# Performance work log

Measured on AMD Instinct MI355X. Metric: run time of the kernel, lower is better.

## Reference

```python
import jax, jax.numpy as jnp
import numpy as np
import math

HID, NH, NKV, HD = 2048, 16, 4, 128
GROUPS = NH // NKV

def fq(x, bits, axis=None):
    # symmetric fake-quant with straight-through rounding; per-tensor unless axis given
    qmax = 2.0 ** (bits - 1) - 1.0
    if axis is None:
        amax = jnp.max(jnp.abs(x))
    else:
        amax = jnp.max(jnp.abs(x), axis=axis, keepdims=True)
    scale = jnp.maximum(amax, 1e-8) / qmax
    q = jnp.clip(jnp.round(x / scale), -qmax - 1.0, qmax) * scale
    return x + jax.lax.stop_gradient(q - x)

def dyn_quant_linear(x, W, b, w_bits=8):
    # DynamicQuantLinear: per-out-channel weight fake-quant + dynamic per-tensor 8-bit act quant
    Wq = fq(W, w_bits, axis=1)          # W: [out, in]
    xq = fq(x, 8)
    y = xq @ Wq.T
    return y + b if b is not None else y

def fq_matmul(a, b, a_bits, b_bits):
    # FakeQuantMatmul
    return jnp.einsum('hqd,hdk->hqk', fq(a, a_bits), fq(b, b_bits))

def rotate_half(x):
    x1, x2 = jnp.split(x, 2, axis=-1)
    return jnp.concatenate([-x2, x1], axis=-1)

def setup_inputs() -> dict:
    key = jax.random.key(0)
    ks = jax.random.split(key, 12)
    inp = {
        'hidden_states': jax.random.normal(ks[0], (1, 512, HID), jnp.float32),
        'cos': jax.random.uniform(ks[1], (1, 512, HD), jnp.float32),
        'sin': jax.random.uniform(ks[2], (1, 512, HD), jnp.float32),
        'cache_k': jax.random.normal(ks[3], (NKV, 8192, HD), jnp.float32),
        'cache_v': jax.random.normal(ks[4], (NKV, 8192, HD), jnp.float32),
        'mask': jnp.zeros((1, 512, 8192), jnp.float32),
        'Wq': jax.random.normal(ks[5], (NH * HD, HID), jnp.float32) * 0.02,
        'bq': jnp.zeros((NH * HD,), jnp.float32),
        'Wk': jax.random.normal(ks[6], (NKV * HD, HID), jnp.float32) * 0.02,
        'bk': jnp.zeros((NKV * HD,), jnp.float32),
        'Wv': jax.random.normal(ks[7], (NKV * HD, HID), jnp.float32) * 0.02,
        'bv': jnp.zeros((NKV * HD,), jnp.float32),
        'Wo': jax.random.normal(ks[8], (HID, NH * HD), jnp.float32) * 0.02,
    }
    return inp

def reference(hidden_states, cos, sin, cache_k, cache_v, mask, Wq, bq, Wk, bk, Wv, bv, Wo):
    # ConstFakeQuant on incoming caches
    cache_k = fq(cache_k, 8)
    cache_v = fq(cache_v, 8)
    seqlen = hidden_states.shape[1]
    x = hidden_states.reshape(seqlen, HID)  # batch_size == 1
    q = dyn_quant_linear(x, Wq, bq).reshape(seqlen, NH, HD).transpose(1, 0, 2)    # [NH,S,D]
    k = dyn_quant_linear(x, Wk, bk).reshape(seqlen, NKV, HD).transpose(1, 0, 2)   # [NKV,S,D]
    v = dyn_quant_linear(x, Wv, bv).reshape(seqlen, NKV, HD).transpose(1, 0, 2)   # [NKV,S,D]
    # RoPE
    q = q * cos + rotate_half(q) * sin
    k = k * cos + rotate_half(k) * sin
    c_len = cache_k.shape[1]
    # sliding KV cache: drop oldest seqlen, append new
    cache_k = jnp.concatenate([cache_k[:, seqlen:, :], k], axis=1)   # [NKV,c_len,D]
    cache_v = jnp.concatenate([cache_v[:, seqlen:, :], v], axis=1)
    kT = cache_k.transpose(0, 2, 1)                                   # [NKV,D,c_len]
    q4 = q.reshape(NKV, GROUPS * seqlen, HD)
    attn = fq_matmul(q4, kT, 8, 8)                                    # [NKV,G*S,c_len]
    attn = attn.reshape(NH, seqlen, c_len) / math.sqrt(HD)
    attn = attn + mask
    attn = jax.nn.softmax(attn, axis=-1)
    attn = attn.reshape(NKV, GROUPS * seqlen, c_len)
    out = fq_matmul(attn, cache_v, 8, 8)                              # sv: [NKV,G*S,D]
    out = out.reshape(NH, seqlen, HD).transpose(1, 0, 2).reshape(1, seqlen, HID)
    out = dyn_quant_linear(out.reshape(seqlen, HID), Wo, None).reshape(1, seqlen, HID)
    # cache outputs re-fake-quantized
    k_out = fq(k, 8)
    v_out = fq(v, 8)
    return (out, k_out, v_out)
```

## Files before the change

kernel.cpp:

```cpp
#include <hip/hip_runtime.h>
#include <math.h>

#define S_LEN 512
#define HID 2048
#define NH 16
#define NKV 4
#define HD 128
#define CL 8192
#define TAILN (CL - S_LEN)
#define NKO (NKV * S_LEN * HD)
#define KS1 16
#define KCH1 (CL / KS1)
#define KS2 8
#define KCH2 (CL / KS2)
#define INV_SQRT_HD 0.08838834764831845f

typedef unsigned short u16;
typedef unsigned int u32;
typedef __attribute__((ext_vector_type(8))) unsigned short u16x8;
typedef __attribute__((ext_vector_type(4))) unsigned short u16x4;
typedef __attribute__((ext_vector_type(8))) short bf16x8;
typedef __attribute__((ext_vector_type(4))) float f32x4;

enum {
  SC_AMAX_X = 0, SC_AMAX_CK, SC_AMAX_CK_TAIL, SC_AMAX_CV, SC_AMAX_CV_TAIL,
  SC_AMAX_Q, SC_AMAX_K, SC_AMAX_V, SC_AMAX_AO, SC_MIN_L,
  SC_NUM
};

__device__ __forceinline__ float warpMax64(float v) {
  #pragma unroll
  for (int o = 32; o; o >>= 1) v = fmaxf(v, __shfl_down(v, o, 64));
  return v;
}
__device__ __forceinline__ float warpMin64(float v) {
  #pragma unroll
  for (int o = 32; o; o >>= 1) v = fminf(v, __shfl_down(v, o, 64));
  return v;
}
__device__ __forceinline__ float blockMax256(float v) {
  __shared__ float sm_[4];
  __syncthreads();
  v = warpMax64(v);
  if ((threadIdx.x & 63) == 0) sm_[threadIdx.x >> 6] = v;
  __syncthreads();
  return fmaxf(fmaxf(sm_[0], sm_[1]), fmaxf(sm_[2], sm_[3]));
}
__device__ __forceinline__ float blockMin256(float v) {
  __shared__ float sn_[4];
  __syncthreads();
  v = warpMin64(v);
  if ((threadIdx.x & 63) == 0) sn_[threadIdx.x >> 6] = v;
  __syncthreads();
  return fminf(fminf(sn_[0], sn_[1]), fminf(sn_[2], sn_[3]));
}
__device__ __forceinline__ void atomicMinPosF(float* a, float v) {
  atomicMin((unsigned int*)a, __float_as_uint(v));
}
__device__ __forceinline__ float clampq(float q) {
  return fminf(fmaxf(q, -128.f), 127.f);
}
__device__ __forceinline__ u16 bf16bits(float f) {
  return (u16)(__float_as_uint(f) >> 16);
}
__device__ __forceinline__ float mk_scale(float am) {
  return fmaxf(am, 1e-8f) / 127.f;
}
__device__ __forceinline__ void gl2lds16(const u16* g, u16* l) {
  __builtin_amdgcn_global_load_lds((const __attribute__((address_space(1))) void*)g,
                                   (__attribute__((address_space(3))) void*)l, 16, 0, 0);
}

__global__ __launch_bounds__(256) void k_pre(const float* __restrict__ hidden,
                                             const float* __restrict__ ck, const float* __restrict__ cv,
                                             float* __restrict__ pp) {
  int b = blockIdx.x, tid = threadIdx.x;
  if (b < 512) {
    const int n4 = S_LEN * HID / 4;
    float m = 0.f;
    const float4* x4 = (const float4*)hidden;
    for (int i = b * 256 + tid; i < n4; i += 512 * 256) {
      float4 v = x4[i];
      m = fmaxf(m, fmaxf(fmaxf(fabsf(v.x), fabsf(v.y)), fmaxf(fabsf(v.z), fabsf(v.w))));
    }
    m = blockMax256(m);
    if (tid == 0) pp[b] = m;
  } else {
    int isv = b >= 1024;
    int bb = b - (isv ? 1024 : 512);
    const float4* x4 = (const float4*)(isv ? cv : ck);
    const int n4 = NKV * CL * HD / 4;
    float mf = 0.f, mt = 0.f;
    for (int i = bb * 256 + tid; i < n4; i += 512 * 256) {
      float4 v = x4[i];
      float a = fmaxf(fmaxf(fabsf(v.x), fabsf(v.y)), fmaxf(fabsf(v.z), fabsf(v.w)));
      mf = fmaxf(mf, a);
      int t = (i >> 5) & (CL - 1);
      if (t >= S_LEN) mt = fmaxf(mt, a);
    }
    mf = blockMax256(mf);
    mt = blockMax256(mt);
    if (tid == 0) {
      pp[512 + isv * 1024 + bb] = mf;
      pp[1024 + isv * 1024 + bb] = mt;
    }
  }
}

__global__ __launch_bounds__(256) void k_reduce_pre(const float* __restrict__ pp, float* __restrict__ sc) {
  const int slots[5] = {SC_AMAX_X, SC_AMAX_CK, SC_AMAX_CK_TAIL, SC_AMAX_CV, SC_AMAX_CV_TAIL};
  if (threadIdx.x == 0) sc[SC_MIN_L] = INFINITY;
  #pragma unroll
  for (int r = 0; r < 5; r++) {
    float v = fmaxf(pp[r * 512 + threadIdx.x], pp[r * 512 + 256 + threadIdx.x]);
    v = blockMax256(v);
    if (threadIdx.x == 0) sc[slots[r]] = v;
  }
}

__global__ __launch_bounds__(256) void k_quant_w_all(const float* __restrict__ Wq, const float* __restrict__ Wk,
                                                     const float* __restrict__ Wv, const float* __restrict__ Wo,
                                                     u16* __restrict__ WQb, u16* __restrict__ WKb,
                                                     u16* __restrict__ WVb, u16* __restrict__ WOb,
                                                     float* __restrict__ SWq, float* __restrict__ SWk,
                                                     float* __restrict__ SWv, float* __restrict__ SWo) {
  int r = blockIdx.x;
  const float* W; u16* Wb; float* SW; int row;
  if (r < 2048)      { W = Wq; Wb = WQb; SW = SWq; row = r; }
  else if (r < 2560) { W = Wk; Wb = WKb; SW = SWk; row = r - 2048; }
  else if (r < 3072) { W = Wv; Wb = WVb; SW = SWv; row = r - 2560; }
  else               { W = Wo; Wb = WOb; SW = SWo; row = r - 3072; }
  size_t base = (size_t)row * HID;
  const float4* w4 = (const float4*)(W + base);
  int tid = threadIdx.x;
  float4 va = w4[tid];
  float4 vb = w4[tid + 256];
  float am = fmaxf(fmaxf(fmaxf(fabsf(va.x), fabsf(va.y)), fmaxf(fabsf(va.z), fabsf(va.w))),
                   fmaxf(fmaxf(fabsf(vb.x), fabsf(vb.y)), fmaxf(fabsf(vb.z), fabsf(vb.w))));
  am = blockMax256(am);
  float s = fmaxf(am, 1e-8f) / 127.f;
  if (tid == 0) SW[row] = s;
  u16x4 oa, ob;
  oa[0] = bf16bits(clampq(rintf(va.x / s)));
  oa[1] = bf16bits(clampq(rintf(va.y / s)));
  oa[2] = bf16bits(clampq(rintf(va.z / s)));
  oa[3] = bf16bits(clampq(rintf(va.w / s)));
  ob[0] = bf16bits(clampq(rintf(vb.x / s)));
  ob[1] = bf16bits(clampq(rintf(vb.y / s)));
  ob[2] = bf16bits(clampq(rintf(vb.z / s)));
  ob[3] = bf16bits(clampq(rintf(vb.w / s)));
  *(u16x4*)(Wb + base + (size_t)tid * 4) = oa;
  *(u16x4*)(Wb + base + (size_t)(tid + 256) * 4) = ob;
}

__global__ __launch_bounds__(256) void k_quant_act_b(const float* __restrict__ in, u16* __restrict__ outp,
                                                     int n4, const float* __restrict__ sc, int axslot) {
  float s = mk_scale(sc[axslot]);
  const float4* i4 = (const float4*)in;
  for (int i = blockIdx.x * 256 + threadIdx.x; i < n4; i += gridDim.x * 256) {
    float4 v = i4[i];
    u16x4 o;
    o[0] = bf16bits(clampq(rintf(v.x / s)));
    o[1] = bf16bits(clampq(rintf(v.y / s)));
    o[2] = bf16bits(clampq(rintf(v.z / s)));
    o[3] = bf16bits(clampq(rintf(v.w / s)));
    *(u16x4*)(outp + (size_t)i * 4) = o;
  }
}

__global__ __launch_bounds__(256) void k_quant_q(const float* __restrict__ QB, u16* __restrict__ QI,
                                                 const float* __restrict__ sc) {
  int idx = blockIdx.x * 256 + threadIdx.x;
  float s = mk_scale(sc[SC_AMAX_Q]);
  int e = idx * 4;
  int srow = e >> 11, rem = e & 2047;
  int h = rem >> 7, d = rem & 127;
  float4 v = *(const float4*)&QB[e];
  u16x4 o;
  o[0] = bf16bits(clampq(rintf(v.x / s)));
  o[1] = bf16bits(clampq(rintf(v.y / s)));
  o[2] = bf16bits(clampq(rintf(v.z / s)));
  o[3] = bf16bits(clampq(rintf(v.w / s)));
  *(u16x4*)(QI + ((size_t)h * S_LEN + srow) * HD + d) = o;
}

#define GQ_STAGE(BUF, K0)                                                          \
  {                                                                                \
    _Pragma("unroll")                                                              \
    for (int i = 0; i < 2; i++) {                                                  \
      int b = tid + i * 256;                                                       \
      int row = b >> 3, c8d = b & 7, c8s = c8d ^ (row & 7);                        \
      gl2lds16(A + (size_t)(r0 + row) * HID + (K0) + c8s * 8, Al[BUF] + b * 8);    \
    }                                                                              \
    _Pragma("unroll")                                                              \
    for (int i = 0; i < 2; i++) {                                                  \
      int b = tid + i * 256;                                                       \
      int row = b >> 3, c8d = b & 7, c8s = c8d ^ (row & 7);                        \
      gl2lds16(B + (size_t)(c0 + row) * HID + (K0) + c8s * 8, Bl[BUF] + b * 8);    \
    }                                                                              \
  }

#define GQ_TILE(BUF)                                                               \
  {                                                                                \
    _Pragma("unroll")                                                              \
    for (int ks = 0; ks < 2; ks++) {                                               \
      bf16x8 af[2], bfr[2];                                                        \
      _Pragma("unroll")                                                            \
      for (int a = 0; a < 2; a++) {                                                \
        int row = wy * 32 + a * 16 + c;                                            \
        af[a] = *(const bf16x8*)(Al[BUF] + row * 64 + (((4 * ks + g) ^ (row & 7)) * 8)); \
      }                                                                            \
      _Pragma("unroll")                                                            \
      for (int b2 = 0; b2 < 2; b2++) {                                             \
        int row = wx * 32 + b2 * 16 + c;                                           \
        bfr[b2] = *(const bf16x8*)(Bl[BUF] + row * 64 + (((4 * ks + g) ^ (row & 7)) * 8)); \
      }                                                                            \
      _Pragma("unroll")                                                            \
      for (int a = 0; a < 2; a++)                                                  \
        _Pragma("unroll")                                                          \
        for (int b2 = 0; b2 < 2; b2++)                                             \
          acc[a][b2] = __builtin_amdgcn_mfma_f32_16x16x32_bf16(af[a], bfr[b2], acc[a][b2], 0, 0, 0); \
    }                                                                              \
  }

__global__ __launch_bounds__(256) void k_gemm_qkv(const u16* __restrict__ A,
                                                  const u16* __restrict__ WQb, const u16* __restrict__ WKb,
                                                  const u16* __restrict__ WVb,
                                                  const float* __restrict__ SWq, const float* __restrict__ SWk,
                                                  const float* __restrict__ SWv,
                                                  const float* __restrict__ bq, const float* __restrict__ bk,
                                                  const float* __restrict__ bv,
                                                  const float* __restrict__ sc,
                                                  float* __restrict__ QB, float* __restrict__ KB,
                                                  float* __restrict__ VB) {
  __shared__ u16 Al[2][64 * 64];
  __shared__ u16 Bl[2][64 * 64];
  int bx = blockIdx.x;
  const u16* B; const float* SW; const float* bias; float* C; int N, c0;
  if (bx < 32)      { B = WQb; SW = SWq; bias = bq; C = QB; N = HID; c0 = bx * 64; }
  else if (bx < 40) { B = WKb; SW = SWk; bias = bk; C = KB; N = NKV * HD; c0 = (bx - 32) * 64; }
  else              { B = WVb; SW = SWv; bias = bv; C = VB; N = NKV * HD; c0 = (bx - 40) * 64; }
  int tid = threadIdx.x, lane = tid & 63, w = tid >> 6;
  int g = lane >> 4, c = lane & 15;
  int wy = w >> 1, wx = w & 1;
  int r0 = blockIdx.y * 64;
  float sx = mk_scale(sc[SC_AMAX_X]);
  f32x4 acc[2][2] = {};
  GQ_STAGE(0, 0)
  __syncthreads();
  for (int k0 = 0; k0 < HID; k0 += 128) {
    GQ_STAGE(1, k0 + 64)
    GQ_TILE(0)
    __syncthreads();
    if (k0 + 128 < HID) GQ_STAGE(0, k0 + 128)
    GQ_TILE(1)
    __syncthreads();
  }
  #pragma unroll
  for (int a = 0; a < 2; a++)
    #pragma unroll
    for (int b2 = 0; b2 < 2; b2++) {
      int col = c0 + wx * 32 + b2 * 16 + c;
      float sca = sx * SW[col];
      float bs = bias[col];
      #pragma unroll
      for (int r = 0; r < 4; r++) {
        int row = r0 + wy * 32 + a * 16 + 4 * g + r;
        C[(size_t)row * N + col] = acc[a][b2][r] * sca + bs;
      }
    }
}

__global__ __launch_bounds__(256) void k_gemm_q(const u16* __restrict__ A, const u16* __restrict__ B,
                                                const float* __restrict__ SW, const float* __restrict__ sc,
                                                int axslot, float* __restrict__ C, int M, int N, int K) {
  __shared__ u16 Al[2][64 * 64];
  __shared__ u16 Bl[2][64 * 64];
  int tid = threadIdx.x, lane = tid & 63, w = tid >> 6;
  int g = lane >> 4, c = lane & 15;
  int wy = w >> 1, wx = w & 1;
  int r0 = blockIdx.y * 64, c0 = blockIdx.x * 64;
  float sx = mk_scale(sc[axslot]);
  f32x4 acc[2][2] = {};
  GQ_STAGE(0, 0)
  __syncthreads();
  for (int k0 = 0; k0 < HID; k0 += 128) {
    GQ_STAGE(1, k0 + 64)
    GQ_TILE(0)
    __syncthreads();
    if (k0 + 128 < HID) GQ_STAGE(0, k0 + 128)
    GQ_TILE(1)
    __syncthreads();
  }
  #pragma unroll
  for (int a = 0; a < 2; a++)
    #pragma unroll
    for (int b2 = 0; b2 < 2; b2++) {
      int col = c0 + wx * 32 + b2 * 16 + c;
      float sca = sx * SW[col];
      #pragma unroll
      for (int r = 0; r < 4; r++) {
        int row = r0 + wy * 32 + a * 16 + 4 * g + r;
        C[(size_t)row * N + col] = acc[a][b2][r] * sca;
      }
    }
}

__global__ __launch_bounds__(256) void k_rope_amax(float* __restrict__ QB, float* __restrict__ KB,
                                                   const float* __restrict__ VB,
                                                   const float* __restrict__ cosb, const float* __restrict__ sinb,
                                                   float* __restrict__ PR) {
  const int nQ = S_LEN * NH * 64;
  const int nK = S_LEN * NKV * 64;
  int idx = blockIdx.x * 256 + threadIdx.x;
  float am = 0.f;
  if (idx < nQ) {
    int s = idx >> 10, rem = idx & 1023, h = rem >> 6, d = rem & 63;
    float c1 = cosb[s * HD + d], s1 = sinb[s * HD + d];
    float c2 = cosb[s * HD + d + 64], s2 = sinb[s * HD + d + 64];
    float* p = &QB[(size_t)s * (NH * HD) + h * HD + d];
    float x1 = p[0], x2 = p[64];
    float y1 = x1 * c1 - x2 * s1;
    float y2 = x2 * c2 + x1 * s2;
    p[0] = y1; p[64] = y2;
    am = fmaxf(fabsf(y1), fabsf(y2));
  } else if (idx < nQ + nK) {
    int j = idx - nQ;
    int s = j >> 8, rem = j & 255, h = rem >> 6, d = rem & 63;
    float c1 = cosb[s * HD + d], s1 = sinb[s * HD + d];
    float c2 = cosb[s * HD + d + 64], s2 = sinb[s * HD + d + 64];
    float* p = &KB[(size_t)s * (NKV * HD) + h * HD + d];
    float x1 = p[0], x2 = p[64];
    float y1 = x1 * c1 - x2 * s1;
    float y2 = x2 * c2 + x1 * s2;
    p[0] = y1; p[64] = y2;
    am = fmaxf(fabsf(y1), fabsf(y2));
  } else {
    int j = idx - nQ - nK;
    float4 v = ((const float4*)VB)[j];
    am = fmaxf(fmaxf(fabsf(v.x), fabsf(v.y)), fmaxf(fabsf(v.z), fabsf(v.w)));
  }
  am = blockMax256(am);
  if (threadIdx.x == 0) PR[blockIdx.x] = am;
}

__global__ __launch_bounds__(256) void k_reduce_rope(const float* __restrict__ PR, float* __restrict__ sc) {
  float v = 0.f;
  #pragma unroll
  for (int i = 0; i < 8; i++) v = fmaxf(v, PR[threadIdx.x + 256 * i]);
  v = blockMax256(v);
  if (threadIdx.x == 0) sc[SC_AMAX_Q] = v;
  v = fmaxf(PR[2048 + threadIdx.x], PR[2048 + 256 + threadIdx.x]);
  v = blockMax256(v);
  if (threadIdx.x == 0) sc[SC_AMAX_K] = v;
  v = PR[2560 + threadIdx.x];
  v = blockMax256(v);
  if (threadIdx.x == 0) sc[SC_AMAX_V] = v;
}

__global__ __launch_bounds__(256) void k_build_cache2(const float* __restrict__ ck, const float* __restrict__ cv,
                                                      const float* __restrict__ KB, const float* __restrict__ VB,
                                                      u16* __restrict__ KCb, u16* __restrict__ VCb,
                                                      u16* __restrict__ VT, float* __restrict__ dout,
                                                      const float* __restrict__ sc) {
  __shared__ u16 T[64][140];
  int b = blockIdx.x;
  int isv = b >= NKV * 128;
  int bb = b - isv * NKV * 128;
  int kvh = bb >> 7, tb = bb & 127;
  float s1 = mk_scale(sc[isv ? SC_AMAX_CV : SC_AMAX_CK]);
  float tq = fminf(rintf(sc[isv ? SC_AMAX_CV_TAIL : SC_AMAX_CK_TAIL] / s1), 127.f) * s1;
  float s2 = fmaxf(fmaxf(tq, sc[isv ? SC_AMAX_V : SC_AMAX_K]), 1e-8f) / 127.f;
  float so = mk_scale(sc[isv ? SC_AMAX_V : SC_AMAX_K]);
  const float* cache = isv ? cv : ck;
  const float* fresh = isv ? VB : KB;
  u16* Cb = isv ? VCb : KCb;
  int tid = threadIdx.x;
  int t0 = tb * 64;
  #pragma unroll
  for (int i = 0; i < 8; i++) {
    int idx = tid + i * 256;
    int t = idx >> 5, d4 = (idx & 31) << 2;
    int tt = t0 + t;
    float4 x;
    float q0_, q1_, q2_, q3_;
    if (tt < TAILN) {
      x = *(const float4*)&cache[((size_t)kvh * CL + tt + S_LEN) * HD + d4];
      q0_ = clampq(rintf(clampq(rintf(x.x / s1)) * s1 / s2));
      q1_ = clampq(rintf(clampq(rintf(x.y / s1)) * s1 / s2));
      q2_ = clampq(rintf(clampq(rintf(x.z / s1)) * s1 / s2));
      q3_ = clampq(rintf(clampq(rintf(x.w / s1)) * s1 / s2));
    } else {
      x = *(const float4*)&fresh[(size_t)(tt - TAILN) * (NKV * HD) + kvh * HD + d4];
      q0_ = clampq(rintf(x.x / s2));
      q1_ = clampq(rintf(x.y / s2));
      q2_ = clampq(rintf(x.z / s2));
      q3_ = clampq(rintf(x.w / s2));
      float4 o;
      o.x = clampq(rintf(x.x / so)) * so;
      o.y = clampq(rintf(x.y / so)) * so;
      o.z = clampq(rintf(x.z / so)) * so;
      o.w = clampq(rintf(x.w / so)) * so;
      *(float4*)&dout[(size_t)S_LEN * HID + (size_t)isv * NKO +
                      ((size_t)kvh * S_LEN + (tt - TAILN)) * HD + d4] = o;
    }
    u16x4 ov;
    ov[0] = bf16bits(q0_); ov[1] = bf16bits(q1_); ov[2] = bf16bits(q2_); ov[3] = bf16bits(q3_);
    *(u16x4*)(Cb + ((size_t)kvh * CL + tt) * HD + d4) = ov;
    if (isv) *(u16x4*)&T[t][d4] = ov;
  }
  if (isv) {
    __syncthreads();
    #pragma unroll
    for (int i = 0; i < 4; i++) {
      int j = tid + i * 256;
      int d = j >> 3, tc = (j & 7) << 3;
      u16x8 v;
      #pragma unroll
      for (int k = 0; k < 8; k++) v[k] = T[tc + k][d];
      *(u16x8*)(VT + ((size_t)kvh * HD + d) * CL + t0 + tc) = v;
    }
  }
}

#define M1_STAGE(BUF, KBASE)                                                       \
  {                                                                                \
    const u16* kgt = Kg + (size_t)(KBASE) * HD;                                    \
    _Pragma("unroll")                                                              \
    for (int i = 0; i < 4; i++) {                                                  \
      int b = tid + i * 256;                                                       \
      int row = b >> 4, c8d = b & 15, c8s = c8d ^ (row & 7);                       \
      gl2lds16(kgt + row * HD + c8s * 8, Kl[BUF] + b * 8);                         \
    }                                                                              \
  }

#define M1_TILE(BUF, KBASE)                                                        \
  {                                                                                \
    const int kbase_ = (KBASE);                                                    \
    f32x4 sc4[4];                                                                  \
    _Pragma("unroll")                                                              \
    for (int kf = 0; kf < 4; kf++) {                                               \
      f32x4 s4 = {0.f, 0.f, 0.f, 0.f};                                             \
      int krow = kf * 16 + c;                                                      \
      _Pragma("unroll")                                                            \
      for (int ds = 0; ds < 4; ds++) {                                             \
        bf16x8 kf8 = *(const bf16x8*)(Kl[BUF] + krow * HD + (((4 * ds + g) ^ (krow & 7)) * 8)); \
        s4 = __builtin_amdgcn_mfma_f32_16x16x32_bf16(qf[ds], kf8, s4, 0, 0, 0);    \
      }                                                                            \
      sc4[kf] = s4;                                                                \
    }                                                                              \
    _Pragma("unroll")                                                              \
    for (int r = 0; r < 4; r++) {                                                  \
      float v0 = fmaf(sc4[0][r], sscale, mrb[r * CL + kbase_ + c]);                \
      float v1 = fmaf(sc4[1][r], sscale, mrb[r * CL + kbase_ + 16 + c]);           \
      float v2 = fmaf(sc4[2][r], sscale, mrb[r * CL + kbase_ + 32 + c]);           \
      float v3 = fmaf(sc4[3][r], sscale, mrb[r * CL + kbase_ + 48 + c]);           \
      float tmax = fmaxf(fmaxf(v0, v1), fmaxf(v2, v3));                            \
      float nm = fmaxf(m[r], tmax);                                                \
      float e0 = __expf(v0 - nm), e1 = __expf(v1 - nm);                            \
      float e2 = __expf(v2 - nm), e3 = __expf(v3 - nm);                            \
      float f = __expf(m[r] - nm);                                                 \
      l[r] = fmaf(l[r], f, (e0 + e1) + (e2 + e3));                                 \
      m[r] = nm;                                                                   \
    }                                                                              \
  }

__global__ __launch_bounds__(256) void k_mattn1(const u16* __restrict__ QI, const u16* __restrict__ KCb,
                                                const float* __restrict__ mask, const float* __restrict__ sc,
                                                float* __restrict__ PM, float* __restrict__ PL) {
  __shared__ u16 Kl[2][64 * HD];
  int bid = blockIdx.x;
  int wki = (bid & 7) * (NH * 8 * KS1 / 8) + (bid >> 3);
  int kc = wki >> 7, rem2 = wki & 127, qb = rem2 >> 4, h = rem2 & 15, kv = h >> 2;
  int tid = threadIdx.x, lane = tid & 63, wv = tid >> 6, g = lane >> 4, c = lane & 15;
  float sq  = mk_scale(sc[SC_AMAX_Q]);
  float sck = mk_scale(sc[SC_AMAX_CK]);
  float tqk = fminf(rintf(sc[SC_AMAX_CK_TAIL] / sck), 127.f) * sck;
  float skn = fmaxf(fmaxf(tqk, sc[SC_AMAX_K]), 1e-8f) / 127.f;
  float sscale = sq * skn * INV_SQRT_HD;
  int q0 = qb * 64 + wv * 16;
  bf16x8 qf[4];
  {
    const u16* qrow = QI + ((size_t)h * S_LEN + q0 + c) * HD + g * 8;
    #pragma unroll
    for (int ds = 0; ds < 4; ds++) qf[ds] = *(const bf16x8*)(qrow + 32 * ds);
  }
  float m[4], l[4];
  #pragma unroll
  for (int r = 0; r < 4; r++) { m[r] = -INFINITY; l[r] = 0.f; }
  int qlane = q0 + 4 * g;
  int kbase0 = kc * KCH1;
  const u16* Kg = KCb + (size_t)kv * CL * HD;
  const float* mrb = mask + (size_t)qlane * CL;
  M1_STAGE(0, kbase0)
  __syncthreads();
  for (int kb = 0; kb < KCH1; kb += 128) {
    M1_STAGE(1, kbase0 + kb + 64)
    M1_TILE(0, kbase0 + kb)
    __syncthreads();
    if (kb + 128 < KCH1) M1_STAGE(0, kbase0 + kb + 128)
    M1_TILE(1, kbase0 + kb + 64)
    __syncthreads();
  }
  #pragma unroll
  for (int r = 0; r < 4; r++) {
    #pragma unroll
    for (int off = 1; off < 16; off <<= 1) {
      float om = __shfl_xor(m[r], off, 64);
      float ol = __shfl_xor(l[r], off, 64);
      float nm = fmaxf(m[r], om);
      l[r] = l[r] * __expf(m[r] - nm) + ol * __expf(om - nm);
      m[r] = nm;
    }
  }
  if (c == 0) {
    size_t base = ((size_t)kc * NH + h) * S_LEN + qlane;
    #pragma unroll
    for (int r = 0; r < 4; r++) { PM[base + r] = m[r]; PL[base + r] = l[r]; }
  }
}

__global__ __launch_bounds__(256) void k_merge4(const float* __restrict__ PM, const float* __restrict__ PL,
                                                float* __restrict__ MLm, float* __restrict__ MLl, float* sc) {
  int idx = blockIdx.x * 256 + threadIdx.x;
  const int st = NH * S_LEN;
  float m = PM[idx];
  #pragma unroll
  for (int p = 1; p < KS1; p++) m = fmaxf(m, PM[p * st + idx]);
  float l = 0.f;
  #pragma unroll
  for (int p = 0; p < KS1; p++) l += PL[p * st + idx] * __expf(PM[p * st + idx] - m);
  MLm[idx] = m; MLl[idx] = l;
  float lm = blockMin256(l);
  if (threadIdx.x == 0) atomicMinPosF(&sc[SC_MIN_L], lm);
}

#define M2_STAGE(BUF, KBASE)                                                       \
  {                                                                                \
    const u16* kgt = Kg + (size_t)(KBASE) * HD;                                    \
    const u16* vgt = Vg + (KBASE);                                                 \
    _Pragma("unroll")                                                              \
    for (int i = 0; i < 4; i++) {                                                  \
      int b = tid + i * 256;                                                       \
      int row = b >> 4, c8d = b & 15, c8s = c8d ^ (row & 7);                       \
      gl2lds16(kgt + row * HD + c8s * 8, Kl[BUF] + b * 8);                         \
    }                                                                              \
    _Pragma("unroll")                                                              \
    for (int i = 0; i < 4; i++) {                                                  \
      int b = tid + i * 256;                                                       \
      int row = b >> 3, c8d = b & 7, c8s = c8d ^ (row & 7);                        \
      gl2lds16(vgt + (size_t)row * CL + c8s * 8, Vl[BUF] + b * 8);                 \
    }                                                                              \
  }

#define M2_TILE(BUF, KBASE)                                                        \
  {                                                                                \
    const int kbase_ = (KBASE);                                                    \
    u32 pw[2][2][4];                  \
    _Pragma("unroll")                                                              \
    for (int kf = 0; kf < 4; kf++) {                                               \
      f32x4 s40 = {0.f, 0.f, 0.f, 0.f}, s41 = {0.f, 0.f, 0.f, 0.f};                \
      int krow = kf * 16 + c;                                                      \
      _Pragma("unroll")                                                            \
      for (int ds = 0; ds < 4; ds++) {                                             \
        bf16x8 kf8 = *(const bf16x8*)(Kl[BUF] + krow * HD + (((4 * ds + g) ^ (krow & 7)) * 8)); \
        s40 = __builtin_amdgcn_mfma_f32_16x16x32_bf16(kf8, qf[0][ds], s40, 0, 0, 0); \
        s41 = __builtin_amdgcn_mfma_f32_16x16x32_bf16(kf8, qf[1][ds], s41, 0, 0, 0); \
      }                                                                            \
      int keyb = kbase_ + kf * 16 + 4 * g;                                         \
      float p0 = fminf(rintf(__expf(fmaf(s40[0], sscale, mrb0[keyb + 0]) - mreg[0]) * cvl[0]), 127.f); \
      float p1 = fminf(rintf(__expf(fmaf(s40[1], sscale, mrb0[keyb + 1]) - mreg[0]) * cvl[0]), 127.f); \
      float p2 = fminf(rintf(__expf(fmaf(s40[2], sscale, mrb0[keyb + 2]) - mreg[0]) * cvl[0]), 127.f); \
      float p3 = fminf(rintf(__expf(fmaf(s40[3], sscale, mrb0[keyb + 3]) - mreg[0]) * cvl[0]), 127.f); \
      pw[0][0][kf] = (u32)bf16bits(p0) | ((u32)bf16bits(p1) << 16);                \
      pw[0][1][kf] = (u32)bf16bits(p2) | ((u32)bf16bits(p3) << 16);                \
      p0 = fminf(rintf(__expf(fmaf(s41[0], sscale, mrb1[keyb + 0]) - mreg[1]) * cvl[1]), 127.f); \
      p1 = fminf(rintf(__expf(fmaf(s41[1], sscale, mrb1[keyb + 1]) - mreg[1]) * cvl[1]), 127.f); \
      p2 = fminf(rintf(__expf(fmaf(s41[2], sscale, mrb1[keyb + 2]) - mreg[1]) * cvl[1]), 127.f); \
      p3 = fminf(rintf(__expf(fmaf(s41[3], sscale, mrb1[keyb + 3]) - mreg[1]) * cvl[1]), 127.f); \
      pw[1][0][kf] = (u32)bf16bits(p0) | ((u32)bf16bits(p1) << 16);                \
      pw[1][1][kf] = (u32)bf16bits(p2) | ((u32)bf16bits(p3) << 16);                \
    }                                                                              \
    int src0 = ((g & 1) * 2) * 16 + c;                                             \
    int src1 = src0 + 16;                                                          \
    int hi = g >> 1;                                                               \
    bf16x8 pa[2][2];                                                               \
    _Pragma("unroll")                                                              \
    for (int s = 0; s < 2; s++) {                                                  \
      _Pragma("unroll")                                                            \
      for (int u = 0; u < 2; u++) {                                                \
        int a0 = __shfl((int)pw[u][0][2 * s], src0, 64);                           \
        int b0 = __shfl((int)pw[u][0][2 * s + 1], src0, 64);                       \
        int a1 = __shfl((int)pw[u][1][2 * s], src0, 64);                           \
        int b1 = __shfl((int)pw[u][1][2 * s + 1], src0, 64);                       \
        int a2 = __shfl((int)pw[u][0][2 * s], src1, 64);                           \
        int b2 = __shfl((int)pw[u][0][2 * s + 1], src1, 64);                       \
        int a3 = __shfl((int)pw[u][1][2 * s], src1, 64);                           \
        int b3 = __shfl((int)pw[u][1][2 * s + 1], src1, 64);                       \
        int4 wv4;                                                                  \
        wv4.x = hi ? b0 : a0; wv4.y = hi ? b1 : a1;                                \
        wv4.z = hi ? b2 : a2; wv4.w = hi ? b3 : a3;                                \
        pa[u][s] = *(bf16x8*)&wv4;                                                 \
      }                                                                            \
    }                                                                              \
    _Pragma("unroll")                                                              \
    for (int dt = 0; dt < 8; dt++) {                                               \
      int drow = dt * 16 + c;                                                      \
      bf16x8 vf0 = *(const bf16x8*)(Vl[BUF] + drow * 64 + ((g ^ (drow & 7)) * 8)); \
      acc[0][dt] = __builtin_amdgcn_mfma_f32_16x16x32_bf16(pa[0][0], vf0, acc[0][dt], 0, 0, 0); \
      acc[1][dt] = __builtin_amdgcn_mfma_f32_16x16x32_bf16(pa[1][0], vf0, acc[1][dt], 0, 0, 0); \
      bf16x8 vf1 = *(const bf16x8*)(Vl[BUF] + drow * 64 + (((4 + g) ^ (drow & 7)) * 8)); \
      acc[0][dt] = __builtin_amdgcn_mfma_f32_16x16x32_bf16(pa[0][1], vf1, acc[0][dt], 0, 0, 0); \
      acc[1][dt] = __builtin_amdgcn_mfma_f32_16x16x32_bf16(pa[1][1], vf1, acc[1][dt], 0, 0, 0); \
    }                                                                              \
  }

__global__ __launch_bounds__(256) void k_mattn2(const u16* __restrict__ QI, const u16* __restrict__ KCb,
                                                const u16* __restrict__ VT, const float* __restrict__ mask,
                                                const float* __restrict__ sc, const float* __restrict__ MLm,
                                                const float* __restrict__ MLl, float* __restrict__ AOp) {
  __shared__ u16 Kl[2][64 * HD];
  __shared__ u16 Vl[2][HD * 64];
  int bid = blockIdx.x;
  int wki = (bid & 7) * (NH * 4 * KS2 / 8) + (bid >> 3);
  int kc = wki >> 6, rem2 = wki & 63, qb = rem2 >> 4, h = rem2 & 15, kv = h >> 2;
  int tid = threadIdx.x, lane = tid & 63, wv = tid >> 6, g = lane >> 4, c = lane & 15;
  float sq  = mk_scale(sc[SC_AMAX_Q]);
  float sck = mk_scale(sc[SC_AMAX_CK]);
  float tqk = fminf(rintf(sc[SC_AMAX_CK_TAIL] / sck), 127.f) * sck;
  float skn = fmaxf(fmaxf(tqk, sc[SC_AMAX_K]), 1e-8f) / 127.f;
  float sscale = sq * skn * INV_SQRT_HD;
  float scv = mk_scale(sc[SC_AMAX_CV]);
  float tqv = fminf(rintf(sc[SC_AMAX_CV_TAIL] / scv), 127.f) * scv;
  float svn = fmaxf(fmaxf(tqv, sc[SC_AMAX_V]), 1e-8f) / 127.f;
  float sp  = mk_scale(1.0f / sc[SC_MIN_L]);
  float rsp = 1.0f / sp;
  float psv = sp * svn;
  int q0 = qb * 128 + wv * 32;
  bf16x8 qf[2][4];
  #pragma unroll
  for (int u = 0; u < 2; u++) {
    const u16* qrow = QI + ((size_t)h * S_LEN + q0 + 16 * u + c) * HD + g * 8;
    #pragma unroll
    for (int ds = 0; ds < 4; ds++) qf[u][ds] = *(const bf16x8*)(qrow + 32 * ds);
  }
  float mreg[2], cvl[2];
  #pragma unroll
  for (int u = 0; u < 2; u++) {
    mreg[u] = MLm[h * S_LEN + q0 + 16 * u + c];
    cvl[u] = rsp / MLl[h * S_LEN + q0 + 16 * u + c];
  }
  const float* mrb0 = mask + (size_t)(q0 + c) * CL;
  const float* mrb1 = mask + (size_t)(q0 + 16 + c) * CL;
  f32x4 acc[2][8] = {};
  const u16* Kg = KCb + (size_t)kv * CL * HD;
  const u16* Vg = VT + (size_t)kv * HD * CL;
  int kbase0 = kc * KCH2;
  M2_STAGE(0, kbase0)
  __syncthreads();
  for (int kb = 0; kb < KCH2; kb += 128) {
    M2_STAGE(1, kbase0 + kb + 64)
    M2_TILE(0, kbase0 + kb)
    __syncthreads();
    if (kb + 128 < KCH2) M2_STAGE(0, kbase0 + kb + 128)
    M2_TILE(1, kbase0 + kb + 64)
    __syncthreads();
  }
  float* outp = AOp + (size_t)kc * S_LEN * HID;
  #pragma unroll
  for (int u = 0; u < 2; u++)
    #pragma unroll
    for (int dt = 0; dt < 8; dt++)
      #pragma unroll
      for (int r = 0; r < 4; r++)
        outp[(size_t)(q0 + 16 * u + 4 * g + r) * HID + h * HD + dt * 16 + c] = acc[u][dt][r] * psv;
}

__global__ __launch_bounds__(256) void k_combine_ao(const float* __restrict__ AOp, float* __restrict__ AO,
                                                    float* __restrict__ PA) {
  int idx = blockIdx.x * 256 + threadIdx.x;
  const int st = S_LEN * HID / 4;
  const f32x4* p4 = (const f32x4*)AOp;
  f32x4 a = p4[idx];
  #pragma unroll
  for (int p = 1; p < KS2; p++) {
    f32x4 b = p4[p * st + idx];
    a = a + b;
  }
  *((f32x4*)AO + idx) = a;
  float am = fmaxf(fmaxf(fabsf(a[0]), fabsf(a[1])), fmaxf(fabsf(a[2]), fabsf(a[3])));
  am = blockMax256(am);
  if (threadIdx.x == 0) PA[blockIdx.x] = am;
}

__global__ __launch_bounds__(256) void k_reduce_ao(const float* __restrict__ PA, float* __restrict__ sc) {
  float v = 0.f;
  #pragma unroll
  for (int i = 0; i < 4; i++) v = fmaxf(v, PA[threadIdx.x + 256 * i]);
  v = blockMax256(v);
  if (threadIdx.x == 0) sc[SC_AMAX_AO] = v;
}

extern "C" void kernel_launch(void* const* d_in, const int* in_sizes, int n_in,
                              void* d_out, int out_size, void* d_ws, size_t ws_size,
                              hipStream_t stream) {
  const float* hidden = (const float*)d_in[0];
  const float* cosb   = (const float*)d_in[1];
  const float* sinb   = (const float*)d_in[2];
  const float* cachek = (const float*)d_in[3];
  const float* cachev = (const float*)d_in[4];
  const float* mask   = (const float*)d_in[5];
  const float* Wq     = (const float*)d_in[6];
  const float* bq     = (const float*)d_in[7];
  const float* Wk     = (const float*)d_in[8];
  const float* bk     = (const float*)d_in[9];
  const float* Wv     = (const float*)d_in[10];
  const float* bv     = (const float*)d_in[11];
  const float* Wo     = (const float*)d_in[12];
  float* out = (float*)d_out;

  char* base = (char*)d_ws;
  auto alloc = [&](size_t bytes) { char* p = base; base += (bytes + 255) & ~(size_t)255; return p; };

  float* SC  = (float*)alloc(64 * 4);
  float* PP  = (float*)alloc(2560 * 4);
  float* PR  = (float*)alloc(2816 * 4);
  float* PA  = (float*)alloc(1024 * 4);
  float* SWq = (float*)alloc(HID * 4);
  float* SWk = (float*)alloc(NKV * HD * 4);
  float* SWv = (float*)alloc(NKV * HD * 4);
  float* SWo = (float*)alloc(HID * 4);
  u16* XI    = (u16*)alloc((size_t)S_LEN * HID * 2);
  u16* WQb   = (u16*)alloc((size_t)HID * HID * 2);
  u16* WKb   = (u16*)alloc((size_t)NKV * HD * HID * 2);
  u16* WVb   = (u16*)alloc((size_t)NKV * HD * HID * 2);
  u16* WOb   = (u16*)alloc((size_t)HID * HID * 2);
  float* QB  = (float*)alloc((size_t)S_LEN * HID * 4);
  float* KB  = (float*)alloc((size_t)S_LEN * NKV * HD * 4);
  float* VB  = (float*)alloc((size_t)S_LEN * NKV * HD * 4);
  u16* KCb   = (u16*)alloc((size_t)NKV * CL * HD * 2);
  u16* VCb   = (u16*)alloc((size_t)NKV * CL * HD * 2);
  u16* VT    = (u16*)alloc((size_t)NKV * HD * CL * 2);
  u16* QI    = (u16*)alloc((size_t)NH * S_LEN * HD * 2);
  float* PM  = (float*)alloc((size_t)KS1 * NH * S_LEN * 4);
  float* PL  = (float*)alloc((size_t)KS1 * NH * S_LEN * 4);
  float* MLm = (float*)alloc((size_t)NH * S_LEN * 4);
  float* MLl = (float*)alloc((size_t)NH * S_LEN * 4);
  float* AOp = (float*)alloc((size_t)KS2 * S_LEN * HID * 4);
  float* AO  = (float*)alloc((size_t)S_LEN * HID * 4);
  u16* AOi   = (u16*)alloc((size_t)S_LEN * HID * 2);

  k_pre<<<1536, 256, 0, stream>>>(hidden, cachek, cachev, PP);
  k_reduce_pre<<<1, 256, 0, stream>>>(PP, SC);
  k_quant_w_all<<<5120, 256, 0, stream>>>(Wq, Wk, Wv, Wo, WQb, WKb, WVb, WOb, SWq, SWk, SWv, SWo);
  k_quant_act_b<<<1024, 256, 0, stream>>>(hidden, XI, S_LEN * HID / 4, SC, SC_AMAX_X);
  {
    dim3 g(48, S_LEN / 64);
    k_gemm_qkv<<<g, 256, 0, stream>>>(XI, WQb, WKb, WVb, SWq, SWk, SWv, bq, bk, bv, SC, QB, KB, VB);
  }
  k_rope_amax<<<2816, 256, 0, stream>>>(QB, KB, VB, cosb, sinb, PR);
  k_reduce_rope<<<1, 256, 0, stream>>>(PR, SC);
  k_build_cache2<<<NKV * 128 * 2, 256, 0, stream>>>(cachek, cachev, KB, VB, KCb, VCb, VT, out, SC);
  k_quant_q<<<1024, 256, 0, stream>>>(QB, QI, SC);
  k_mattn1<<<NH * 8 * KS1, 256, 0, stream>>>(QI, KCb, mask, SC, PM, PL);
  k_merge4<<<NH * S_LEN / 256, 256, 0, stream>>>(PM, PL, MLm, MLl, SC);
  k_mattn2<<<NH * 4 * KS2, 256, 0, stream>>>(QI, KCb, VT, mask, SC, MLm, MLl, AOp);
  k_combine_ao<<<1024, 256, 0, stream>>>(AOp, AO, PA);
  k_reduce_ao<<<1, 256, 0, stream>>>(PA, SC);
  k_quant_act_b<<<1024, 256, 0, stream>>>(AO, AOi, S_LEN * HID / 4, SC, SC_AMAX_AO);
  {
    dim3 g(HID / 64, S_LEN / 64);
    k_gemm_q<<<g, 256, 0, stream>>>(AOi, WOb, SWo, SC, SC_AMAX_AO, out, S_LEN, HID, HID);
  }
  (void)in_sizes; (void)n_in; (void)out_size; (void)ws_size;
}
```

Before: 211.2 us.

## Restructure softmax-stats pass to process 32 query rows per wave with transposed MFMA

The first attention pass (row max and sum) now has each wave handle 32 query rows instead of 16. It swaps MFMA operand order so keys sit on the row dimension, which lets mask values be read as contiguous float4 loads, and it reduces across lane groups instead of columns. This halves the block count and doubles the reuse of each staged K tile in LDS. The second pass's mask reads are also vectorised to float4. The trade-off is higher register pressure and fewer blocks to spread across the CUs.

```diff
diff --git a/kernel.cpp b/kernel.cpp
--- a/kernel.cpp
+++ b/kernel.cpp
@@ -437,126 +437,6 @@
 #define M1_TILE(BUF, KBASE)                                                        \
   {                                                                                \
     const int kbase_ = (KBASE);                                                    \
-    f32x4 sc4[4];                                                                  \
-    _Pragma("unroll")                                                              \
-    for (int kf = 0; kf < 4; kf++) {                                               \
-      f32x4 s4 = {0.f, 0.f, 0.f, 0.f};                                             \
-      int krow = kf * 16 + c;                                                      \
-      _Pragma("unroll")                                                            \
-      for (int ds = 0; ds < 4; ds++) {                                             \
-        bf16x8 kf8 = *(const bf16x8*)(Kl[BUF] + krow * HD + (((4 * ds + g) ^ (krow & 7)) * 8)); \
-        s4 = __builtin_amdgcn_mfma_f32_16x16x32_bf16(qf[ds], kf8, s4, 0, 0, 0);    \
-      }                                                                            \
-      sc4[kf] = s4;                                                                \
-    }                                                                              \
-    _Pragma("unroll")                                                              \
-    for (int r = 0; r < 4; r++) {                                                  \
-      float v0 = fmaf(sc4[0][r], sscale, mrb[r * CL + kbase_ + c]);                \
-      float v1 = fmaf(sc4[1][r], sscale, mrb[r * CL + kbase_ + 16 + c]);           \
-      float v2 = fmaf(sc4[2][r], sscale, mrb[r * CL + kbase_ + 32 + c]);           \
-      float v3 = fmaf(sc4[3][r], sscale, mrb[r * CL + kbase_ + 48 + c]);           \
-      float tmax = fmaxf(fmaxf(v0, v1), fmaxf(v2, v3));                            \
-      float nm = fmaxf(m[r], tmax);                                                \
-      float e0 = __expf(v0 - nm), e1 = __expf(v1 - nm);                            \
-      float e2 = __expf(v2 - nm), e3 = __expf(v3 - nm);                            \
-      float f = __expf(m[r] - nm);                                                 \
-      l[r] = fmaf(l[r], f, (e0 + e1) + (e2 + e3));                                 \
-      m[r] = nm;                                                                   \
-    }                                                                              \
-  }
-
-__global__ __launch_bounds__(256) void k_mattn1(const u16* __restrict__ QI, const u16* __restrict__ KCb,
-                                                const float* __restrict__ mask, const float* __restrict__ sc,
-                                                float* __restrict__ PM, float* __restrict__ PL) {
-  __shared__ u16 Kl[2][64 * HD];
-  int bid = blockIdx.x;
-  int wki = (bid & 7) * (NH * 8 * KS1 / 8) + (bid >> 3);
-  int kc = wki >> 7, rem2 = wki & 127, qb = rem2 >> 4, h = rem2 & 15, kv = h >> 2;
-  int tid = threadIdx.x, lane = tid & 63, wv = tid >> 6, g = lane >> 4, c = lane & 15;
-  float sq  = mk_scale(sc[SC_AMAX_Q]);
-  float sck = mk_scale(sc[SC_AMAX_CK]);
-  float tqk = fminf(rintf(sc[SC_AMAX_CK_TAIL] / sck), 127.f) * sck;
-  float skn = fmaxf(fmaxf(tqk, sc[SC_AMAX_K]), 1e-8f) / 127.f;
-  float sscale = sq * skn * INV_SQRT_HD;
-  int q0 = qb * 64 + wv * 16;
-  bf16x8 qf[4];
-  {
-    const u16* qrow = QI + ((size_t)h * S_LEN + q0 + c) * HD + g * 8;
-    #pragma unroll
-    for (int ds = 0; ds < 4; ds++) qf[ds] = *(const bf16x8*)(qrow + 32 * ds);
-  }
-  float m[4], l[4];
-  #pragma unroll
-  for (int r = 0; r < 4; r++) { m[r] = -INFINITY; l[r] = 0.f; }
-  int qlane = q0 + 4 * g;
-  int kbase0 = kc * KCH1;
-  const u16* Kg = KCb + (size_t)kv * CL * HD;
-  const float* mrb = mask + (size_t)qlane * CL;
-  M1_STAGE(0, kbase0)
-  __syncthreads();
-  for (int kb = 0; kb < KCH1; kb += 128) {
-    M1_STAGE(1, kbase0 + kb + 64)
-    M1_TILE(0, kbase0 + kb)
-    __syncthreads();
-    if (kb + 128 < KCH1) M1_STAGE(0, kbase0 + kb + 128)
-    M1_TILE(1, kbase0 + kb + 64)
-    __syncthreads();
-  }
-  #pragma unroll
-  for (int r = 0; r < 4; r++) {
-    #pragma unroll
-    for (int off = 1; off < 16; off <<= 1) {
-      float om = __shfl_xor(m[r], off, 64);
-      float ol = __shfl_xor(l[r], off, 64);
-      float nm = fmaxf(m[r], om);
-      l[r] = l[r] * __expf(m[r] - nm) + ol * __expf(om - nm);
-      m[r] = nm;
-    }
-  }
-  if (c == 0) {
-    size_t base = ((size_t)kc * NH + h) * S_LEN + qlane;
-    #pragma unroll
-    for (int r = 0; r < 4; r++) { PM[base + r] = m[r]; PL[base + r] = l[r]; }
-  }
-}
-
-__global__ __launch_bounds__(256) void k_merge4(const float* __restrict__ PM, const float* __restrict__ PL,
-                                                float* __restrict__ MLm, float* __restrict__ MLl, float* sc) {
-  int idx = blockIdx.x * 256 + threadIdx.x;
-  const int st = NH * S_LEN;
-  float m = PM[idx];
-  #pragma unroll
-  for (int p = 1; p < KS1; p++) m = fmaxf(m, PM[p * st + idx]);
-  float l = 0.f;
-  #pragma unroll
-  for (int p = 0; p < KS1; p++) l += PL[p * st + idx] * __expf(PM[p * st + idx] - m);
-  MLm[idx] = m; MLl[idx] = l;
-  float lm = blockMin256(l);
-  if (threadIdx.x == 0) atomicMinPosF(&sc[SC_MIN_L], lm);
-}
-
-#define M2_STAGE(BUF, KBASE)                                                       \
-  {                                                                                \
-    const u16* kgt = Kg + (size_t)(KBASE) * HD;                                    \
-    const u16* vgt = Vg + (KBASE);                                                 \
-    _Pragma("unroll")                                                              \
-    for (int i = 0; i < 4; i++) {                                                  \
-      int b = tid + i * 256;                                                       \
-      int row = b >> 4, c8d = b & 15, c8s = c8d ^ (row & 7);                       \
-      gl2lds16(kgt + row * HD + c8s * 8, Kl[BUF] + b * 8);                         \
-    }                                                                              \
-    _Pragma("unroll")                                                              \
-    for (int i = 0; i < 4; i++) {                                                  \
-      int b = tid + i * 256;                                                       \
-      int row = b >> 3, c8d = b & 7, c8s = c8d ^ (row & 7);                        \
-      gl2lds16(vgt + (size_t)row * CL + c8s * 8, Vl[BUF] + b * 8);                 \
-    }                                                                              \
-  }
-
-#define M2_TILE(BUF, KBASE)                                                        \
-  {                                                                                \
-    const int kbase_ = (KBASE);                                                    \
-    u32 pw[2][2][4];                  \
     _Pragma("unroll")                                                              \
     for (int kf = 0; kf < 4; kf++) {                                               \
       f32x4 s40 = {0.f, 0.f, 0.f, 0.f}, s41 = {0.f, 0.f, 0.f, 0.f};                \
@@ -568,16 +448,145 @@
         s41 = __builtin_amdgcn_mfma_f32_16x16x32_bf16(kf8, qf[1][ds], s41, 0, 0, 0); \
       }                                                                            \
       int keyb = kbase_ + kf * 16 + 4 * g;                                         \
-      float p0 = fminf(rintf(__expf(fmaf(s40[0], sscale, mrb0[keyb + 0]) - mreg[0]) * cvl[0]), 127.f); \
-      float p1 = fminf(rintf(__expf(fmaf(s40[1], sscale, mrb0[keyb + 1]) - mreg[0]) * cvl[0]), 127.f); \
-      float p2 = fminf(rintf(__expf(fmaf(s40[2], sscale, mrb0[keyb + 2]) - mreg[0]) * cvl[0]), 127.f); \
-      float p3 = fminf(rintf(__expf(fmaf(s40[3], sscale, mrb0[keyb + 3]) - mreg[0]) * cvl[0]), 127.f); \
+      float4 mv0 = *(const float4*)&mrb0[keyb];                                    \
+      float v0 = fmaf(s40[0], sscale, mv0.x);                                      \
+      float v1 = fmaf(s40[1], sscale, mv0.y);                                      \
+      float v2 = fmaf(s40[2], sscale, mv0.z);                                      \
+      float v3 = fmaf(s40[3], sscale, mv0.w);                                      \
+      float tmax = fmaxf(fmaxf(v0, v1), fmaxf(v2, v3));                            \
+      float nm = fmaxf(m[0], tmax);                                                \
+      float e0 = __expf(v0 - nm), e1 = __expf(v1 - nm);                            \
+      float e2 = __expf(v2 - nm), e3 = __expf(v3 - nm);                            \
+      l[0] = fmaf(l[0], __expf(m[0] - nm), (e0 + e1) + (e2 + e3));                 \
+      m[0] = nm;                                                                   \
+      float4 mv1 = *(const float4*)&mrb1[keyb];                                    \
+      v0 = fmaf(s41[0], sscale, mv1.x);                                            \
+      v1 = fmaf(s41[1], sscale, mv1.y);                                            \
+      v2 = fmaf(s41[2], sscale, mv1.z);                                            \
+      v3 = fmaf(s41[3], sscale, mv1.w);                                            \
+      tmax = fmaxf(fmaxf(v0, v1), fmaxf(v2, v3));                                  \
+      nm = fmaxf(m[1], tmax);                                                      \
+      e0 = __expf(v0 - nm); e1 = __expf(v1 - nm);                                  \
+      e2 = __expf(v2 - nm); e3 = __expf(v3 - nm);                                  \
+      l[1] = fmaf(l[1], __expf(m[1] - nm), (e0 + e1) + (e2 + e3));                 \
+      m[1] = nm;                                                                   \
+    }                                                                              \
+  }
+
+__global__ __launch_bounds__(256) void k_mattn1(const u16* __restrict__ QI, const u16* __restrict__ KCb,
+                                                const float* __restrict__ mask, const float* __restrict__ sc,
+                                                float* __restrict__ PM, float* __restrict__ PL) {
+  __shared__ u16 Kl[2][64 * HD];
+  int bid = blockIdx.x;
+  int wki = (bid & 7) * (NH * 4 * KS1 / 8) + (bid >> 3);
+  int kc = wki >> 6, rem2 = wki & 63, qb = rem2 >> 4, h = rem2 & 15, kv = h >> 2;
+  int tid = threadIdx.x, lane = tid & 63, wv = tid >> 6, g = lane >> 4, c = lane & 15;
+  float sq  = mk_scale(sc[SC_AMAX_Q]);
+  float sck = mk_scale(sc[SC_AMAX_CK]);
+  float tqk = fminf(rintf(sc[SC_AMAX_CK_TAIL] / sck), 127.f) * sck;
+  float skn = fmaxf(fmaxf(tqk, sc[SC_AMAX_K]), 1e-8f) / 127.f;
+  float sscale = sq * skn * INV_SQRT_HD;
+  int q0 = qb * 128 + wv * 32;
+  bf16x8 qf[2][4];
+  #pragma unroll
+  for (int u = 0; u < 2; u++) {
+    const u16* qrow = QI + ((size_t)h * S_LEN + q0 + 16 * u + c) * HD + g * 8;
+    #pragma unroll
+    for (int ds = 0; ds < 4; ds++) qf[u][ds] = *(const bf16x8*)(qrow + 32 * ds);
+  }
+  float m[2] = {-INFINITY, -INFINITY}, l[2] = {0.f, 0.f};
+  const float* mrb0 = mask + (size_t)(q0 + c) * CL;
+  const float* mrb1 = mask + (size_t)(q0 + 16 + c) * CL;
+  int kbase0 = kc * KCH1;
+  const u16* Kg = KCb + (size_t)kv * CL * HD;
+  M1_STAGE(0, kbase0)
+  __syncthreads();
+  for (int kb = 0; kb < KCH1; kb += 128) {
+    M1_STAGE(1, kbase0 + kb + 64)
+    M1_TILE(0, kbase0 + kb)
+    __syncthreads();
+    if (kb + 128 < KCH1) M1_STAGE(0, kbase0 + kb + 128)
+    M1_TILE(1, kbase0 + kb + 64)
+    __syncthreads();
+  }
+  #pragma unroll
+  for (int u = 0; u < 2; u++) {
+    #pragma unroll
+    for (int off = 16; off < 64; off <<= 1) {
+      float om = __shfl_xor(m[u], off, 64);
+      float ol = __shfl_xor(l[u], off, 64);
+      float nm = fmaxf(m[u], om);
+      l[u] = l[u] * __expf(m[u] - nm) + ol * __expf(om - nm);
+      m[u] = nm;
+    }
+  }
+  if (g == 0) {
+    size_t base = ((size_t)kc * NH + h) * S_LEN + q0;
+    PM[base + c] = m[0]; PL[base + c] = l[0];
+    PM[base + 16 + c] = m[1]; PL[base + 16 + c] = l[1];
+  }
+}
+
+__global__ __launch_bounds__(256) void k_merge4(const float* __restrict__ PM, const float* __restrict__ PL,
+                                                float* __restrict__ MLm, float* __restrict__ MLl, float* sc) {
+  int idx = blockIdx.x * 256 + threadIdx.x;
+  const int st = NH * S_LEN;
+  float m = PM[idx];
+  #pragma unroll
+  for (int p = 1; p < KS1; p++) m = fmaxf(m, PM[p * st + idx]);
+  float l = 0.f;
+  #pragma unroll
+  for (int p = 0; p < KS1; p++) l += PL[p * st + idx] * __expf(PM[p * st + idx] - m);
+  MLm[idx] = m; MLl[idx] = l;
+  float lm = blockMin256(l);
+  if (threadIdx.x == 0) atomicMinPosF(&sc[SC_MIN_L], lm);
+}
+
+#define M2_STAGE(BUF, KBASE)                                                       \
+  {                                                                                \
+    const u16* kgt = Kg + (size_t)(KBASE) * HD;                                    \
+    const u16* vgt = Vg + (KBASE);                                                 \
+    _Pragma("unroll")                                                              \
+    for (int i = 0; i < 4; i++) {                                                  \
+      int b = tid + i * 256;                                                       \
+      int row = b >> 4, c8d = b & 15, c8s = c8d ^ (row & 7);                       \
+      gl2lds16(kgt + row * HD + c8s * 8, Kl[BUF] + b * 8);                         \
+    }                                                                              \
+    _Pragma("unroll")                                                              \
+    for (int i = 0; i < 4; i++) {                                                  \
+      int b = tid + i * 256;                                                       \
+      int row = b >> 3, c8d = b & 7, c8s = c8d ^ (row & 7);                        \
+      gl2lds16(vgt + (size_t)row * CL + c8s * 8, Vl[BUF] + b * 8);                 \
+    }                                                                              \
+  }
+
+#define M2_TILE(BUF, KBASE)                                                        \
+  {                                                                                \
+    const int kbase_ = (KBASE);                                                    \
+    u32 pw[2][2][4];                  \
+    _Pragma("unroll")                                                              \
+    for (int kf = 0; kf < 4; kf++) {                                               \
+      f32x4 s40 = {0.f, 0.f, 0.f, 0.f}, s41 = {0.f, 0.f, 0.f, 0.f};                \
+      int krow = kf * 16 + c;                                                      \
+      _Pragma("unroll")                                                            \
+      for (int ds = 0; ds < 4; ds++) {                                             \
+        bf16x8 kf8 = *(const bf16x8*)(Kl[BUF] + krow * HD + (((4 * ds + g) ^ (krow & 7)) * 8)); \
+        s40 = __builtin_amdgcn_mfma_f32_16x16x32_bf16(kf8, qf[0][ds], s40, 0, 0, 0); \
+        s41 = __builtin_amdgcn_mfma_f32_16x16x32_bf16(kf8, qf[1][ds], s41, 0, 0, 0); \
+      }                                                                            \
+      int keyb = kbase_ + kf * 16 + 4 * g;                                         \
+      float4 mv0 = *(const float4*)&mrb0[keyb];                                    \
+      float p0 = fminf(rintf(__expf(fmaf(s40[0], sscale, mv0.x) - mreg[0]) * cvl[0]), 127.f); \
+      float p1 = fminf(rintf(__expf(fmaf(s40[1], sscale, mv0.y) - mreg[0]) * cvl[0]), 127.f); \
+      float p2 = fminf(rintf(__expf(fmaf(s40[2], sscale, mv0.z) - mreg[0]) * cvl[0]), 127.f); \
+      float p3 = fminf(rintf(__expf(fmaf(s40[3], sscale, mv0.w) - mreg[0]) * cvl[0]), 127.f); \
       pw[0][0][kf] = (u32)bf16bits(p0) | ((u32)bf16bits(p1) << 16);                \
       pw[0][1][kf] = (u32)bf16bits(p2) | ((u32)bf16bits(p3) << 16);                \
-      p0 = fminf(rintf(__expf(fmaf(s41[0], sscale, mrb1[keyb + 0]) - mreg[1]) * cvl[1]), 127.f); \
-      p1 = fminf(rintf(__expf(fmaf(s41[1], sscale, mrb1[keyb + 1]) - mreg[1]) * cvl[1]), 127.f); \
-      p2 = fminf(rintf(__expf(fmaf(s41[2], sscale, mrb1[keyb + 2]) - mreg[1]) * cvl[1]), 127.f); \
-      p3 = fminf(rintf(__expf(fmaf(s41[3], sscale, mrb1[keyb + 3]) - mreg[1]) * cvl[1]), 127.f); \
+      float4 mv1 = *(const float4*)&mrb1[keyb];                                    \
+      p0 = fminf(rintf(__expf(fmaf(s41[0], sscale, mv1.x) - mreg[1]) * cvl[1]), 127.f); \
+      p1 = fminf(rintf(__expf(fmaf(s41[1], sscale, mv1.y) - mreg[1]) * cvl[1]), 127.f); \
+      p2 = fminf(rintf(__expf(fmaf(s41[2], sscale, mv1.z) - mreg[1]) * cvl[1]), 127.f); \
+      p3 = fminf(rintf(__expf(fmaf(s41[3], sscale, mv1.w) - mreg[1]) * cvl[1]), 127.f); \
       pw[1][0][kf] = (u32)bf16bits(p0) | ((u32)bf16bits(p1) << 16);                \
       pw[1][1][kf] = (u32)bf16bits(p2) | ((u32)bf16bits(p3) << 16);                \
     }                                                                              \
@@ -762,7 +771,7 @@
   k_reduce_rope<<<1, 256, 0, stream>>>(PR, SC);
   k_build_cache2<<<NKV * 128 * 2, 256, 0, stream>>>(cachek, cachev, KB, VB, KCb, VCb, VT, out, SC);
   k_quant_q<<<1024, 256, 0, stream>>>(QB, QI, SC);
-  k_mattn1<<<NH * 8 * KS1, 256, 0, stream>>>(QI, KCb, mask, SC, PM, PL);
+  k_mattn1<<<NH * 4 * KS1, 256, 0, stream>>>(QI, KCb, mask, SC, PM, PL);
   k_merge4<<<NH * S_LEN / 256, 256, 0, stream>>>(PM, PL, MLm, MLl, SC);
   k_mattn2<<<NH * 4 * KS2, 256, 0, stream>>>(QI, KCb, VT, mask, SC, MLm, MLl, AOp);
   k_combine_ao<<<1024, 256, 0, stream>>>(AOp, AO, PA);
```

Result: slower. 218.4 us (+3.4%).
